# Optimization experiments

Hardware: AMD Instinct MI355X
Metric: run time of the kernel (lower is better)

Reference implementation:

```python
import jax, jax.numpy as jnp
import numpy as np

DIM = 1024
ATT_DIM = 1024
NUM_HEADS = 16
HEAD_DIM = ATT_DIM // NUM_HEADS


def setup_inputs() -> dict:
    key = jax.random.key(0)
    ks = jax.random.split(key, 13)
    s = lambda fan_in: 1.0 / np.sqrt(fan_in)
    bsz, n = 8, 1024
    x = jax.random.normal(ks[0], (bsz, n, DIM), dtype=jnp.float32)
    # Linear weights stored as [in, out] (apply via x @ W + b)
    Wq = jax.random.uniform(ks[1], (DIM, ATT_DIM), minval=-s(DIM), maxval=s(DIM))
    bq = jax.random.uniform(ks[2], (ATT_DIM,), minval=-s(DIM), maxval=s(DIM))
    Wk = jax.random.uniform(ks[3], (DIM, ATT_DIM), minval=-s(DIM), maxval=s(DIM))
    bk = jax.random.uniform(ks[4], (ATT_DIM,), minval=-s(DIM), maxval=s(DIM))
    Wv = jax.random.uniform(ks[5], (DIM, ATT_DIM), minval=-s(DIM), maxval=s(DIM))
    bv = jax.random.uniform(ks[6], (ATT_DIM,), minval=-s(DIM), maxval=s(DIM))
    Win = jax.random.uniform(ks[7], (DIM, HEAD_DIM), minval=-s(DIM), maxval=s(DIM))
    bin_ = jax.random.uniform(ks[8], (HEAD_DIM,), minval=-s(DIM), maxval=s(DIM))
    d_in1 = HEAD_DIM * (NUM_HEADS + 1)
    W1 = jax.random.uniform(ks[9], (d_in1, 2 * DIM), minval=-s(d_in1), maxval=s(d_in1))
    b1 = jax.random.uniform(ks[10], (2 * DIM,), minval=-s(d_in1), maxval=s(d_in1))
    W2 = jax.random.uniform(ks[11], (2 * DIM, DIM), minval=-s(2 * DIM), maxval=s(2 * DIM))
    b2 = jax.random.uniform(ks[12], (DIM,), minval=-s(2 * DIM), maxval=s(2 * DIM))
    return {"x": x, "Wq": Wq, "bq": bq, "Wk": Wk, "bk": bk, "Wv": Wv, "bv": bv,
            "Win": Win, "bin_": bin_, "W1": W1, "b1": b1, "W2": W2, "b2": b2}


def reference(x, Wq, bq, Wk, bk, Wv, bv, Win, bin_, W1, b1, W2, b2):
    bsz, n, _ = x.shape
    scaling = HEAD_DIM ** (-0.5)
    # [b, n, h, d]
    q = (x @ Wq + bq).reshape(bsz, n, NUM_HEADS, HEAD_DIM) * scaling
    k = (x @ Wk + bk).reshape(bsz, n, NUM_HEADS, HEAD_DIM)
    v = (x @ Wv + bv).reshape(bsz, n, NUM_HEADS, HEAD_DIM)
    # scores [b, h, n, n]
    score = jnp.einsum('bihd,bjhd->bhij', q, k)
    diag = jnp.eye(n, dtype=bool)  # self positions masked with -inf
    score = jnp.where(diag[None, None], -jnp.inf, score)
    attn = jax.nn.softmax(score, axis=-1)
    out = jnp.einsum('bhij,bjhd->bihd', attn, v).reshape(bsz, n, NUM_HEADS * HEAD_DIM)
    in_ = (x @ Win + bin_)  # [b, n, head_dim]
    out = jnp.concatenate([out, in_], axis=-1)
    h = jax.nn.relu(out @ W1 + b1)
    return h @ W2 + b2
```

## Files before the change

### kernel.cpp

```cpp
#include <hip/hip_runtime.h>

typedef __bf16 bf16;
typedef __attribute__((ext_vector_type(8))) __bf16 bf16x8;
typedef __attribute__((ext_vector_type(4))) __bf16 bf16x4;
typedef __attribute__((ext_vector_type(4))) short short4_t;
typedef __attribute__((ext_vector_type(4))) float floatx4;

typedef const void __attribute__((address_space(1)))* gas1p;
typedef void __attribute__((address_space(3)))* las3p;

#define LOG2E 1.44269504088896340736f

static constexpr int D_MODEL = 1024;
static constexpr int N_HEADS = 16;
static constexpr int HDIM    = 64;
static constexpr int BSZ     = 8;
static constexpr int SEQ     = 1024;
static constexpr int ROWS    = BSZ * SEQ;
static constexpr int FF_IN   = 1088;
static constexpr int FF_HID  = 2048;
static constexpr int QKV_LD  = 3072;

__device__ __forceinline__ floatx4 mfma_bf16(bf16x8 a, bf16x8 b, floatx4 c) {
  return __builtin_amdgcn_mfma_f32_16x16x32_bf16(a, b, c, 0, 0, 0);
}

__device__ __forceinline__ floatx4 mfma16(bf16x4 a, bf16x4 b, floatx4 c) {
#if __has_builtin(__builtin_amdgcn_mfma_f32_16x16x16_bf16)
  return __builtin_amdgcn_mfma_f32_16x16x16_bf16(a, b, c, 0, 0, 0);
#else
  return __builtin_amdgcn_mfma_f32_16x16x16bf16_1k(
      __builtin_bit_cast(short4_t, a), __builtin_bit_cast(short4_t, b), c, 0, 0, 0);
#endif
}

__device__ __forceinline__ float flex_load(const void* src, size_t idx, int isbf) {
  return isbf ? (float)((const bf16*)src)[idx] : ((const float*)src)[idx];
}

__global__ void detect_kernel(const unsigned* __restrict__ w, int* __restrict__ flag) {
  __shared__ int cnt;
  if (threadIdx.x == 0) cnt = 0;
  __syncthreads();
  int hits = 0;
  for (int i = threadIdx.x; i < 4096; i += 256) {
    const unsigned v = w[(size_t)i * 997 + 13];
    const unsigned b = (v >> 8) & 0x7F;
    hits += (b >= 0x3B && b <= 0x41) ? 1 : 0;
  }
  atomicAdd(&cnt, hits);
  __syncthreads();
  if (threadIdx.x == 0) *flag = (cnt > 2048) ? 1 : 0;
}

__global__ __launch_bounds__(256)
void x_to_bf16_kernel(const void* __restrict__ src, bf16* __restrict__ dst,
                      const int* __restrict__ flag) {
  const int isbf = *flag;
  const size_t i = ((size_t)blockIdx.x * 256 + threadIdx.x) * 8;
  bf16x8 o;
  if (isbf) {
    o = *reinterpret_cast<const bf16x8*>((const bf16*)src + i);
  } else {
    const float4 f0 = *reinterpret_cast<const float4*>((const float*)src + i);
    const float4 f1 = *reinterpret_cast<const float4*>((const float*)src + i + 4);
    o[0] = (bf16)f0.x; o[1] = (bf16)f0.y; o[2] = (bf16)f0.z; o[3] = (bf16)f0.w;
    o[4] = (bf16)f1.x; o[5] = (bf16)f1.y; o[6] = (bf16)f1.z; o[7] = (bf16)f1.w;
  }
  *reinterpret_cast<bf16x8*>(dst + i) = o;
}

__global__ __launch_bounds__(256)
void bias_all_kernel(const void* bq, const void* bk, const void* bv,
                     const void* bin, const void* b1, const void* b2,
                     float* __restrict__ dst, const int* __restrict__ flag) {
  const int isbf = *flag;
  const int i = blockIdx.x * 256 + threadIdx.x;
  if (i < 1024)      dst[i] = flex_load(bq, i, isbf) * 0.125f;
  else if (i < 2048) dst[i] = flex_load(bk, i - 1024, isbf);
  else if (i < 3072) dst[i] = flex_load(bv, i - 2048, isbf);
  else if (i < 3136) dst[i] = flex_load(bin, i - 3072, isbf);
  else if (i < 5184) dst[i] = flex_load(b1, i - 3136, isbf);
  else if (i < 6208) dst[i] = flex_load(b2, i - 5184, isbf);
}

struct TransJobs {
  const void* src[6];
  bf16* dst[6];
  int R[6], C[6];
  int tiles_x[6];
  int tile_base[7];
  float scale[6];
};

__global__ __launch_bounds__(256)
void transpose_all_kernel(TransJobs J, const int* __restrict__ flag) {
  __shared__ float tile[32][33];
  const int isbf = *flag;
  const int bid = blockIdx.x;
  int j = 0;
#pragma unroll
  for (int t = 1; t < 6; t++) j += (bid >= J.tile_base[t]) ? 1 : 0;
  const int t = bid - J.tile_base[j];
  const int c0 = (t % J.tiles_x[j]) * 32, r0 = (t / J.tiles_x[j]) * 32;
  const void* src = J.src[j];
  bf16* dst = J.dst[j];
  const int R = J.R[j], C = J.C[j];
  const float scale = J.scale[j];
  const int tx = threadIdx.x & 31, ty = threadIdx.x >> 5;
  for (int i = ty; i < 32; i += 8)
    tile[i][tx] = flex_load(src, (size_t)(r0 + i) * C + (c0 + tx), isbf);
  __syncthreads();
  for (int i = ty; i < 32; i += 8)
    dst[(size_t)(c0 + i) * R + (r0 + tx)] = (bf16)(tile[tx][i] * scale);
}

__global__ __launch_bounds__(256)
void transpose_v_kernel(const bf16* __restrict__ v, bf16* __restrict__ vt) {
  __shared__ float tile[32][33];
  const int bh = blockIdx.z, b = bh >> 4, h = bh & 15;
  const int s0 = blockIdx.x * 32, d0 = blockIdx.y * 32;
  const int tx = threadIdx.x & 31, ty = threadIdx.x >> 5;
  const bf16* src = v + (size_t)b * SEQ * QKV_LD + 2048 + h * HDIM;
  bf16* dst = vt + (size_t)bh * HDIM * SEQ;
  for (int i = ty; i < 32; i += 8)
    tile[i][tx] = (float)src[(size_t)(s0 + i) * QKV_LD + d0 + tx];
  __syncthreads();
  for (int i = ty; i < 32; i += 8)
    dst[(size_t)(d0 + i) * SEQ + s0 + tx] = (bf16)tile[tx][i];
}

template <int BN, bool DO_RELU, bool OUT_FLEX>
__global__ __launch_bounds__(256)
void gemm_bt(const bf16* __restrict__ A, const bf16* __restrict__ BT,
             const float* __restrict__ bias,
             void* __restrict__ Cv, int N, int K, int ldc,
             bf16* __restrict__ C2, int ldc2, int nsplit, int nvalid,
             const int* __restrict__ flag) {
  constexpr int BM = 128, BK = 64;
  constexpr int TCN = BN / 32;
  constexpr int ACH = (BM * BK) / (256 * 8);
  constexpr int BCH = (BN * BK) / (256 * 8);
  __shared__ bf16 As[BM * BK];
  __shared__ bf16 Bs[BN * BK];
  const int tid = threadIdx.x;
  const int wave = tid >> 6, lane = tid & 63;
  const int quad = lane >> 4, lo = lane & 15;
  const int wm = wave >> 1, wn = wave & 1;
  const int m0 = blockIdx.x * BM;
  const int n0 = blockIdx.y * BN;

  floatx4 acc[4][TCN];
#pragma unroll
  for (int i = 0; i < 4; i++)
#pragma unroll
    for (int j = 0; j < TCN; j++) acc[i][j] = floatx4{0.f, 0.f, 0.f, 0.f};

  for (int kb = 0; kb < K; kb += BK) {
#pragma unroll
    for (int u = 0; u < ACH; u++) {
      const int c = u * 256 + tid;
      const int row = c >> 3, col = c & 7;
      const int gcol = col ^ (row & 7);
      const bf16* g = A + (size_t)(m0 + row) * K + kb + gcol * 8;
      __builtin_amdgcn_global_load_lds((gas1p)g, (las3p)(As + c * 8), 16, 0, 0);
    }
#pragma unroll
    for (int u = 0; u < BCH; u++) {
      const int c = u * 256 + tid;
      const int row = c >> 3, col = c & 7;
      const int gcol = col ^ (row & 7);
      const bf16* g = BT + (size_t)(n0 + row) * K + kb + gcol * 8;
      __builtin_amdgcn_global_load_lds((gas1p)g, (las3p)(Bs + c * 8), 16, 0, 0);
    }
    __syncthreads();
#pragma unroll
    for (int kk = 0; kk < 2; kk++) {
      bf16x8 af[4], bfr[TCN];
#pragma unroll
      for (int tr = 0; tr < 4; tr++) {
        const int row = wm * 64 + tr * 16 + lo;
        const int cc = (kk * 4 + quad) ^ (lo & 7);
        af[tr] = *reinterpret_cast<const bf16x8*>(As + row * BK + cc * 8);
      }
#pragma unroll
      for (int tc = 0; tc < TCN; tc++) {
        const int row = wn * (BN / 2) + tc * 16 + lo;
        const int cc = (kk * 4 + quad) ^ (lo & 7);
        bfr[tc] = *reinterpret_cast<const bf16x8*>(Bs + row * BK + cc * 8);
      }
#pragma unroll
      for (int tr = 0; tr < 4; tr++)
#pragma unroll
        for (int tc = 0; tc < TCN; tc++)
          acc[tr][tc] = mfma_bf16(af[tr], bfr[tc], acc[tr][tc]);
    }
    __syncthreads();
  }

  const int isbf = OUT_FLEX ? *flag : 1;
#pragma unroll
  for (int tc = 0; tc < TCN; tc++) {
    const int col = n0 + wn * (BN / 2) + tc * 16 + lo;
    const float bval = bias[col];
    if (col < nsplit) {
#pragma unroll
      for (int tr = 0; tr < 4; tr++) {
        const int rbase = m0 + wm * 64 + tr * 16 + quad * 4;
#pragma unroll
        for (int r = 0; r < 4; r++) {
          float v = acc[tr][tc][r] + bval;
          if (DO_RELU) v = fmaxf(v, 0.f);
          const size_t idx = (size_t)(rbase + r) * ldc + col;
          if (!OUT_FLEX || isbf) ((bf16*)Cv)[idx] = (bf16)v;
          else                   ((float*)Cv)[idx] = v;
        }
      }
    } else if (col < nvalid) {
#pragma unroll
      for (int tr = 0; tr < 4; tr++) {
        const int rbase = m0 + wm * 64 + tr * 16 + quad * 4;
#pragma unroll
        for (int r = 0; r < 4; r++) {
          float v = acc[tr][tc][r] + bval;
          if (DO_RELU) v = fmaxf(v, 0.f);
          C2[(size_t)(rbase + r) * ldc2 + (col - nsplit)] = (bf16)v;
        }
      }
    }
  }
}

__global__ __launch_bounds__(256)
void attn_kernel(const bf16* __restrict__ QKV, const bf16* __restrict__ Vt,
                 bf16* __restrict__ Cc) {
  __shared__ bf16 Ks[64 * 64];
  __shared__ bf16 Vs[64 * 64];
  const int bid = blockIdx.x;
  const int xcd = bid & 7, g = bid >> 3;
  const int ib = g & 7, bh = (g >> 3) * 8 + xcd;
  const int b = bh >> 4, h = bh & 15;
  const int i0 = ib * 128;
  const int tid = threadIdx.x, wave = tid >> 6, lane = tid & 63;
  const int quad = lane >> 4, lo = lane & 15;
  const int iw = i0 + wave * 32;
  const bf16* qptr = QKV + (size_t)b * SEQ * QKV_LD + h * HDIM;
  const bf16* kptr = QKV + (size_t)b * SEQ * QKV_LD + 1024 + h * HDIM;
  const bf16* vptr = Vt + (size_t)bh * HDIM * SEQ;

  bf16x8 qf[2][2];
#pragma unroll
  for (int it = 0; it < 2; it++)
#pragma unroll
    for (int kf = 0; kf < 2; kf++)
      qf[it][kf] = *reinterpret_cast<const bf16x8*>(
          qptr + (size_t)(iw + it * 16 + lo) * QKV_LD + kf * 32 + quad * 8);

  floatx4 oacc[2][4];
  float lrow[2] = {0.f, 0.f};
#pragma unroll
  for (int it = 0; it < 2; it++)
#pragma unroll
    for (int dt = 0; dt < 4; dt++) oacc[it][dt] = floatx4{0.f, 0.f, 0.f, 0.f};

  for (int jb = 0; jb < SEQ / 64; jb++) {
    const int j0 = jb * 64;
#pragma unroll
    for (int u = 0; u < 2; u++) {
      const int c = u * 256 + tid;
      const int row = c >> 3, col = c & 7;
      const int gcol = col ^ (row & 7);
      __builtin_amdgcn_global_load_lds(
          (gas1p)(kptr + (size_t)(j0 + row) * QKV_LD + gcol * 8),
          (las3p)(Ks + c * 8), 16, 0, 0);
      __builtin_amdgcn_global_load_lds(
          (gas1p)(vptr + (size_t)row * SEQ + j0 + gcol * 8),
          (las3p)(Vs + c * 8), 16, 0, 0);
    }
    __syncthreads();

    floatx4 sacc[2][4];
#pragma unroll
    for (int it = 0; it < 2; it++)
#pragma unroll
      for (int mt = 0; mt < 4; mt++) sacc[it][mt] = floatx4{0.f, 0.f, 0.f, 0.f};
#pragma unroll
    for (int mt = 0; mt < 4; mt++) {
      const int r = mt * 16 + lo;
      const int cc0 = quad ^ (lo & 7);
      const int cc1 = (4 + quad) ^ (lo & 7);
      const bf16x8 k0 = *reinterpret_cast<const bf16x8*>(Ks + r * 64 + cc0 * 8);
      const bf16x8 k1 = *reinterpret_cast<const bf16x8*>(Ks + r * 64 + cc1 * 8);
#pragma unroll
      for (int it = 0; it < 2; it++) {
        sacc[it][mt] = mfma_bf16(k0, qf[it][0], sacc[it][mt]);
        sacc[it][mt] = mfma_bf16(k1, qf[it][1], sacc[it][mt]);
      }
    }

    if (j0 == (iw & ~63)) {
#pragma unroll
      for (int it = 0; it < 2; it++) {
        const int ig = iw + it * 16 + lo;
#pragma unroll
        for (int mt = 0; mt < 4; mt++)
#pragma unroll
          for (int r = 0; r < 4; r++)
            if (j0 + mt * 16 + quad * 4 + r == ig) sacc[it][mt][r] = -1e30f;
      }
    }

    bf16x4 pfrag[2][4];
#pragma unroll
    for (int it = 0; it < 2; it++) {
      float s = 0.f;
#pragma unroll
      for (int mt = 0; mt < 4; mt++) {
        bf16x4 pk;
#pragma unroll
        for (int r = 0; r < 4; r++) {
          const float p = exp2f(sacc[it][mt][r] * LOG2E);
          s += p;
          pk[r] = (bf16)p;
        }
        pfrag[it][mt] = pk;
      }
      s += __shfl_xor(s, 16);
      s += __shfl_xor(s, 32);
      lrow[it] += s;
    }

#pragma unroll
    for (int dt = 0; dt < 4; dt++) {
      const int r = dt * 16 + lo;
#pragma unroll
      for (int kt = 0; kt < 4; kt++) {
        const int gch = kt * 2 + (quad >> 1);
        const int cc = gch ^ (lo & 7);
        const bf16x4 vf = *reinterpret_cast<const bf16x4*>(
            Vs + r * 64 + cc * 8 + (quad & 1) * 4);
#pragma unroll
        for (int it = 0; it < 2; it++)
          oacc[it][dt] = mfma16(vf, pfrag[it][kt], oacc[it][dt]);
      }
    }
    __syncthreads();
  }

#pragma unroll
  for (int it = 0; it < 2; it++) {
    const int ig = iw + it * 16 + lo;
    const float inv = 1.0f / lrow[it];
    bf16* cb = Cc + ((size_t)b * SEQ + ig) * FF_IN + h * HDIM;
#pragma unroll
    for (int dt = 0; dt < 4; dt++) {
      bf16x4 o;
#pragma unroll
      for (int r = 0; r < 4; r++) o[r] = (bf16)(oacc[it][dt][r] * inv);
      *reinterpret_cast<bf16x4*>(cb + dt * 16 + quad * 4) = o;
    }
  }
}

extern "C" void kernel_launch(void* const* d_in, const int* in_sizes, int n_in,
                              void* d_out, int out_size, void* d_ws, size_t ws_size,
                              hipStream_t stream) {
  (void)in_sizes; (void)n_in; (void)out_size; (void)ws_size;
  const void* x   = d_in[0];
  const void* Wq  = d_in[1];
  const void* bq  = d_in[2];
  const void* Wk  = d_in[3];
  const void* bk  = d_in[4];
  const void* Wv  = d_in[5];
  const void* bv  = d_in[6];
  const void* Win = d_in[7];
  const void* bin = d_in[8];
  const void* W1  = d_in[9];
  const void* b1  = d_in[10];
  const void* W2  = d_in[11];
  const void* b2  = d_in[12];

  size_t off = 0;
  char* wsb = (char*)d_ws;
  auto alloc = [&](size_t bytes) {
    void* p = (void*)(wsb + off);
    off += (bytes + 255) & ~(size_t)255;
    return p;
  };
  int*   flag  = (int*)alloc(4);
  bf16*  xbf   = (bf16*)alloc((size_t)ROWS * D_MODEL * 2);
  bf16*  WqkvT = (bf16*)alloc((size_t)3200 * 1024 * 2);
  bf16*  W1T   = (bf16*)alloc((size_t)FF_HID * FF_IN * 2);
  bf16*  W2T   = (bf16*)alloc((size_t)D_MODEL * FF_HID * 2);
  float* biasf = (float*)alloc(6208 * 4);
  bf16*  qkv   = (bf16*)alloc((size_t)ROWS * QKV_LD * 2);
  bf16*  vtb   = (bf16*)alloc((size_t)ROWS * D_MODEL * 2);
  bf16*  cbuf  = (bf16*)alloc((size_t)ROWS * FF_IN * 2);
  bf16*  hbuf  = (bf16*)alloc((size_t)ROWS * FF_HID * 2);
  float* b1f   = biasf + 3136;
  float* b2f   = biasf + 5184;

  const dim3 blk(256);
  detect_kernel<<<1, blk, 0, stream>>>((const unsigned*)x, flag);

  x_to_bf16_kernel<<<(ROWS * D_MODEL) / 2048, blk, 0, stream>>>(x, xbf, flag);
  bias_all_kernel<<<25, blk, 0, stream>>>(bq, bk, bv, bin, b1, b2, biasf, flag);

  TransJobs J;
  J.src[0] = Wq;  J.dst[0] = WqkvT;                        J.R[0] = 1024; J.C[0] = 1024; J.scale[0] = 0.125f;
  J.src[1] = Wk;  J.dst[1] = WqkvT + (size_t)1024 * 1024;  J.R[1] = 1024; J.C[1] = 1024; J.scale[1] = 1.0f;
  J.src[2] = Wv;  J.dst[2] = WqkvT + (size_t)2048 * 1024;  J.R[2] = 1024; J.C[2] = 1024; J.scale[2] = 1.0f;
  J.src[3] = Win; J.dst[3] = WqkvT + (size_t)3072 * 1024;  J.R[3] = 1024; J.C[3] = 64;   J.scale[3] = 1.0f;
  J.src[4] = W1;  J.dst[4] = W1T;                          J.R[4] = 1088; J.C[4] = 2048; J.scale[4] = 1.0f;
  J.src[5] = W2;  J.dst[5] = W2T;                          J.R[5] = 2048; J.C[5] = 1024; J.scale[5] = 1.0f;
  int base = 0;
  for (int j = 0; j < 6; j++) {
    J.tiles_x[j] = J.C[j] / 32;
    J.tile_base[j] = base;
    base += (J.R[j] / 32) * (J.C[j] / 32);
  }
  J.tile_base[6] = base;
  transpose_all_kernel<<<base, blk, 0, stream>>>(J, flag);

  gemm_bt<128, false, false><<<dim3(ROWS / 128, 25), blk, 0, stream>>>(
      xbf, WqkvT, biasf, qkv, 3200, 1024, QKV_LD,
      cbuf + 1024, FF_IN, 3072, 3136, nullptr);

  transpose_v_kernel<<<dim3(SEQ / 32, HDIM / 32, BSZ * N_HEADS), blk, 0, stream>>>(qkv, vtb);

  attn_kernel<<<dim3(1024), blk, 0, stream>>>(qkv, vtb, cbuf);

  gemm_bt<128, true, false><<<dim3(ROWS / 128, FF_HID / 128), blk, 0, stream>>>(
      cbuf, W1T, b1f, hbuf, FF_HID, FF_IN, FF_HID,
      nullptr, 0, FF_HID, FF_HID, nullptr);
  gemm_bt<128, false, true><<<dim3(ROWS / 128, D_MODEL / 128), blk, 0, stream>>>(
      hbuf, W2T, b2f, d_out, D_MODEL, FF_HID, D_MODEL,
      nullptr, 0, D_MODEL, D_MODEL, flag);
}
```

Before: 398.3 us.

## Fuse V transpose into QKV GEMM epilogue, fold log2e into Q, add setprio

The QKV GEMM epilogue now writes the V columns directly in transposed per-head layout, staging them through shared memory. This removes the separate transpose_v kernel and its extra read and write of V. The log2(e) factor is folded into the Q weight and bias scaling, so the attention softmax calls exp2 without a multiply. The attention row sum is split into two accumulators, and the MFMA phases are wrapped in s_setprio to favour matrix issue. V blocks now skip the normal qkv store, and the smem epilogue reuses the tile buffer with only a waitcnt, no barrier, which relies on each wave using its own region.

```diff
diff --git a/kernel.cpp b/kernel.cpp
--- a/kernel.cpp
+++ b/kernel.cpp
@@ -76,7 +76,7 @@
                      float* __restrict__ dst, const int* __restrict__ flag) {
   const int isbf = *flag;
   const int i = blockIdx.x * 256 + threadIdx.x;
-  if (i < 1024)      dst[i] = flex_load(bq, i, isbf) * 0.125f;
+  if (i < 1024)      dst[i] = flex_load(bq, i, isbf) * (0.125f * LOG2E);
   else if (i < 2048) dst[i] = flex_load(bk, i - 1024, isbf);
   else if (i < 3072) dst[i] = flex_load(bv, i - 2048, isbf);
   else if (i < 3136) dst[i] = flex_load(bin, i - 3072, isbf);
@@ -115,34 +115,20 @@
     dst[(size_t)(c0 + i) * R + (r0 + tx)] = (bf16)(tile[tx][i] * scale);
 }
 
-__global__ __launch_bounds__(256)
-void transpose_v_kernel(const bf16* __restrict__ v, bf16* __restrict__ vt) {
-  __shared__ float tile[32][33];
-  const int bh = blockIdx.z, b = bh >> 4, h = bh & 15;
-  const int s0 = blockIdx.x * 32, d0 = blockIdx.y * 32;
-  const int tx = threadIdx.x & 31, ty = threadIdx.x >> 5;
-  const bf16* src = v + (size_t)b * SEQ * QKV_LD + 2048 + h * HDIM;
-  bf16* dst = vt + (size_t)bh * HDIM * SEQ;
-  for (int i = ty; i < 32; i += 8)
-    tile[i][tx] = (float)src[(size_t)(s0 + i) * QKV_LD + d0 + tx];
-  __syncthreads();
-  for (int i = ty; i < 32; i += 8)
-    dst[(size_t)(d0 + i) * SEQ + s0 + tx] = (bf16)tile[tx][i];
-}
-
-template <int BN, bool DO_RELU, bool OUT_FLEX>
+template <int BN, bool DO_RELU, bool OUT_FLEX, bool V_TRANS>
 __global__ __launch_bounds__(256)
 void gemm_bt(const bf16* __restrict__ A, const bf16* __restrict__ BT,
              const float* __restrict__ bias,
              void* __restrict__ Cv, int N, int K, int ldc,
              bf16* __restrict__ C2, int ldc2, int nsplit, int nvalid,
-             const int* __restrict__ flag) {
+             bf16* __restrict__ vt_out, const int* __restrict__ flag) {
   constexpr int BM = 128, BK = 64;
   constexpr int TCN = BN / 32;
   constexpr int ACH = (BM * BK) / (256 * 8);
   constexpr int BCH = (BN * BK) / (256 * 8);
-  __shared__ bf16 As[BM * BK];
-  __shared__ bf16 Bs[BN * BK];
+  __shared__ __align__(16) char smem_raw[(BM * BK + BN * BK) * 2];
+  bf16* As = (bf16*)smem_raw;
+  bf16* Bs = As + BM * BK;
   const int tid = threadIdx.x;
   const int wave = tid >> 6, lane = tid & 63;
   const int quad = lane >> 4, lo = lane & 15;
@@ -196,6 +182,37 @@
           acc[tr][tc] = mfma_bf16(af[tr], bfr[tc], acc[tr][tc]);
     }
     __syncthreads();
+  }
+
+  if (V_TRANS && n0 >= 2048 && n0 < 3072) {
+    const int h = ((n0 - 2048) >> 6) + wn;
+    const int b = m0 >> 10;
+    const int ibase = (m0 & 1023) + wm * 64;
+    bf16* L = ((bf16*)smem_raw) + wave * 4096;
+#pragma unroll
+    for (int tc = 0; tc < TCN; tc++) {
+      const int d = tc * 16 + lo;
+      const float bval = bias[n0 + wn * 64 + d];
+#pragma unroll
+      for (int tr = 0; tr < 4; tr++) {
+        const int iin = tr * 16 + quad * 4;
+        bf16x4 p;
+#pragma unroll
+        for (int r = 0; r < 4; r++) p[r] = (bf16)(acc[tr][tc][r] + bval);
+        *reinterpret_cast<bf16x4*>(L + d * 64 + (iin ^ ((d & 7) << 3))) = p;
+      }
+    }
+    asm volatile("s_waitcnt lgkmcnt(0)" ::: "memory");
+    bf16* dst = vt_out + (size_t)(b * 16 + h) * (HDIM * SEQ) + ibase;
+#pragma unroll
+    for (int w8 = 0; w8 < 8; w8++) {
+      const int dp = w8 * 8 + (lane >> 3);
+      const int ip = (lane & 7) * 8;
+      const bf16x8 v = *reinterpret_cast<const bf16x8*>(
+          L + dp * 64 + (ip ^ ((dp & 7) << 3)));
+      *reinterpret_cast<bf16x8*>(dst + (size_t)dp * SEQ + ip) = v;
+    }
+    return;
   }
 
   const int isbf = OUT_FLEX ? *flag : 1;
@@ -284,6 +301,7 @@
     for (int it = 0; it < 2; it++)
 #pragma unroll
       for (int mt = 0; mt < 4; mt++) sacc[it][mt] = floatx4{0.f, 0.f, 0.f, 0.f};
+    __builtin_amdgcn_s_setprio(1);
 #pragma unroll
     for (int mt = 0; mt < 4; mt++) {
       const int r = mt * 16 + lo;
@@ -297,6 +315,7 @@
         sacc[it][mt] = mfma_bf16(k1, qf[it][1], sacc[it][mt]);
       }
     }
+    __builtin_amdgcn_s_setprio(0);
 
     if (j0 == (iw & ~63)) {
 #pragma unroll
@@ -313,23 +332,25 @@
     bf16x4 pfrag[2][4];
 #pragma unroll
     for (int it = 0; it < 2; it++) {
-      float s = 0.f;
+      float s0 = 0.f, s1 = 0.f;
 #pragma unroll
       for (int mt = 0; mt < 4; mt++) {
         bf16x4 pk;
 #pragma unroll
         for (int r = 0; r < 4; r++) {
-          const float p = exp2f(sacc[it][mt][r] * LOG2E);
-          s += p;
+          const float p = exp2f(sacc[it][mt][r]);
+          if (mt & 1) s1 += p; else s0 += p;
           pk[r] = (bf16)p;
         }
         pfrag[it][mt] = pk;
       }
+      float s = s0 + s1;
       s += __shfl_xor(s, 16);
       s += __shfl_xor(s, 32);
       lrow[it] += s;
     }
 
+    __builtin_amdgcn_s_setprio(1);
 #pragma unroll
     for (int dt = 0; dt < 4; dt++) {
       const int r = dt * 16 + lo;
@@ -344,6 +365,7 @@
           oacc[it][dt] = mfma16(vf, pfrag[it][kt], oacc[it][dt]);
       }
     }
+    __builtin_amdgcn_s_setprio(0);
     __syncthreads();
   }
 
@@ -407,7 +429,7 @@
   bias_all_kernel<<<25, blk, 0, stream>>>(bq, bk, bv, bin, b1, b2, biasf, flag);
 
   TransJobs J;
-  J.src[0] = Wq;  J.dst[0] = WqkvT;                        J.R[0] = 1024; J.C[0] = 1024; J.scale[0] = 0.125f;
+  J.src[0] = Wq;  J.dst[0] = WqkvT;                        J.R[0] = 1024; J.C[0] = 1024; J.scale[0] = 0.125f * LOG2E;
   J.src[1] = Wk;  J.dst[1] = WqkvT + (size_t)1024 * 1024;  J.R[1] = 1024; J.C[1] = 1024; J.scale[1] = 1.0f;
   J.src[2] = Wv;  J.dst[2] = WqkvT + (size_t)2048 * 1024;  J.R[2] = 1024; J.C[2] = 1024; J.scale[2] = 1.0f;
   J.src[3] = Win; J.dst[3] = WqkvT + (size_t)3072 * 1024;  J.R[3] = 1024; J.C[3] = 64;   J.scale[3] = 1.0f;
@@ -422,18 +444,16 @@
   J.tile_base[6] = base;
   transpose_all_kernel<<<base, blk, 0, stream>>>(J, flag);
 
-  gemm_bt<128, false, false><<<dim3(ROWS / 128, 25), blk, 0, stream>>>(
+  gemm_bt<128, false, false, true><<<dim3(ROWS / 128, 25), blk, 0, stream>>>(
       xbf, WqkvT, biasf, qkv, 3200, 1024, QKV_LD,
-      cbuf + 1024, FF_IN, 3072, 3136, nullptr);
-
-  transpose_v_kernel<<<dim3(SEQ / 32, HDIM / 32, BSZ * N_HEADS), blk, 0, stream>>>(qkv, vtb);
+      cbuf + 1024, FF_IN, 3072, 3136, vtb, nullptr);
 
   attn_kernel<<<dim3(1024), blk, 0, stream>>>(qkv, vtb, cbuf);
 
-  gemm_bt<128, true, false><<<dim3(ROWS / 128, FF_HID / 128), blk, 0, stream>>>(
+  gemm_bt<128, true, false, false><<<dim3(ROWS / 128, FF_HID / 128), blk, 0, stream>>>(
       cbuf, W1T, b1f, hbuf, FF_HID, FF_IN, FF_HID,
-      nullptr, 0, FF_HID, FF_HID, nullptr);
-  gemm_bt<128, false, true><<<dim3(ROWS / 128, D_MODEL / 128), blk, 0, stream>>>(
+      nullptr, 0, FF_HID, FF_HID, nullptr, nullptr);
+  gemm_bt<128, false, true, false><<<dim3(ROWS / 128, D_MODEL / 128), blk, 0, stream>>>(
       hbuf, W2T, b2f, d_out, D_MODEL, FF_HID, D_MODEL,
-      nullptr, 0, D_MODEL, D_MODEL, flag);
-}
+      nullptr, 0, D_MODEL, D_MODEL, nullptr, flag);
+}
```

Result: faster. 381.0 us (-4.4%).
